# Performance work log

Hardware: AMD Instinct MI355X
Metric: run time of the kernel (lower is better)

The kernel has to match this reference:

```python
import jax, jax.numpy as jnp
import numpy as np

N = 2000
E = 20000
C = 16
B = 128
N_IN = 200   # first N_IN nodes are input nodes
N_OUT = 200  # last N_OUT nodes are output nodes
EPS = 1e-5


def setup_inputs() -> dict:
    key = jax.random.key(0)
    ks = jax.random.split(key, 8)
    x = jax.random.normal(ks[0], (B, N), dtype=jnp.float32)
    edge_index = jax.random.randint(ks[1], (2, E), 0, N, dtype=jnp.int32)
    input_node_mask = jnp.arange(N) < N_IN
    output_node_mask = jnp.arange(N) >= (N - N_OUT)
    func_mask = ~(input_node_mask | output_node_mask)
    # sparse-linear parameters (structured forms of W1/W2/W3)
    w1 = jax.random.normal(ks[2], (E, C), dtype=jnp.float32) * (1.0 / np.sqrt(C))
    b1 = jnp.zeros((N, C), dtype=jnp.float32)
    w2 = jax.random.normal(ks[3], (N, C, C), dtype=jnp.float32) * (1.0 / np.sqrt(C))
    b2 = jnp.zeros((N, C), dtype=jnp.float32)
    w3 = jax.random.normal(ks[4], (E, C), dtype=jnp.float32) * 1.0  # d=1 init scale
    b3 = jnp.zeros((E,), dtype=jnp.float32)
    g1 = jnp.ones((N * C,), dtype=jnp.float32)
    be1 = jnp.zeros((N * C,), dtype=jnp.float32)
    g2 = jnp.ones((N * C,), dtype=jnp.float32)
    be2 = jnp.zeros((N * C,), dtype=jnp.float32)
    return {"x": x, "w1": w1, "b1": b1, "w2": w2, "b2": b2, "w3": w3, "b3": b3,
            "g1": g1, "be1": be1, "g2": g2, "be2": be2,
            "edge_index": edge_index, "func_mask": func_mask,
            "output_node_mask": output_node_mask, "layers": 4}


def _batchnorm(h, g, b):
    # training-mode BatchNorm1d: batch mean and biased variance over axis 0
    m = h.mean(axis=0)
    v = h.var(axis=0)
    return (h - m) * jax.lax.rsqrt(v + EPS) * g + b


def reference(x, w1, b1, w2, b2, w3, b3, g1, be1, g2, be2,
              edge_index, func_mask, output_node_mask, layers):
    src, dst = edge_index[0], edge_index[1]
    Bsz, Nn = x.shape
    Ee, Cc = w1.shape
    fm = func_mask.astype(x.dtype)
    w2m = w2 * fm[:, None, None]          # W2 blocks exist only at function nodes
    w3m = w3 * fm[src][:, None]           # W3 rows exist only for edges with src in function nodes

    x0 = x[:, src]                        # node2edge: (B, E)
    xe = x0
    for _ in range(layers):
        # lin1: scatter edge values into dst node hidden channels
        contrib = xe.T[:, :, None] * w1[:, None, :]                    # (E, B, C)
        h = jax.ops.segment_sum(contrib, dst, num_segments=Nn)         # (N, B, C)
        h = jnp.transpose(h, (1, 0, 2)) + b1                           # (B, N, C)
        h = _batchnorm(h.reshape(Bsz, Nn * Cc), g1, be1)
        h = jax.nn.elu(h).reshape(Bsz, Nn, Cc)
        # lin2: block-diagonal C x C mix per (function) node
        h = jnp.einsum('bnc,ncd->bnd', h, w2m) + b2
        h = _batchnorm(h.reshape(Bsz, Nn * Cc), g2, be2)
        h = jax.nn.elu(h).reshape(Bsz, Nn, Cc)
        # lin3: gather src hidden, per-edge dot back to edge space
        xe = jnp.einsum('bec,ec->be', h[:, src], w3m) + b3             # (B, E)
        xe = xe + x0
    # edge2node: scatter-sum edge values to dst nodes, keep output nodes
    nodes = jax.ops.segment_sum(xe.T, dst, num_segments=Nn)            # (N, B)
    return nodes.T * output_node_mask.astype(x.dtype)
```

## Files before the change

kernel.cpp:

```cpp
#include <hip/hip_runtime.h>
#include <math.h>

#define BB 128
#define NN 2000
#define EE 20000
#define CC 16
#define FUNC_LO 200
#define FUNC_HI 1800
#define OUT_LO 1800
#define LAYERS 4
#define EPSV 1e-5f
#define CH 32
#define HP 129


__global__ void k_hist2(const int* __restrict__ ei, int* __restrict__ deg) {
    int e = blockIdx.x * 256 + threadIdx.x;
    if (e < EE) {
        atomicAdd(&deg[ei[EE + e]], 1);
        atomicAdd(&deg[NN + ei[e]], 1);
    }
}

__global__ void k_scan(const int* __restrict__ deg, int* __restrict__ rs,
                       int* __restrict__ cursor) {
    const int PER = 16;
    int tid = threadIdx.x;
    int vals[PER];
    int s = 0;
    #pragma unroll
    for (int i = 0; i < PER; i++) {
        int idx = tid * PER + i;
        int d = (idx < 2 * NN) ? deg[idx] : 0;
        vals[i] = s;
        s += d;
    }
    __shared__ int ts[256];
    ts[tid] = s;
    __syncthreads();
    for (int off = 1; off < 256; off <<= 1) {
        int v = (tid >= off) ? ts[tid - off] : 0;
        __syncthreads();
        ts[tid] += v;
        __syncthreads();
    }
    int base = (tid == 0) ? 0 : ts[tid - 1];
    #pragma unroll
    for (int i = 0; i < PER; i++) {
        int idx = tid * PER + i;
        if (idx < 2 * NN) {
            int v = base + vals[i];
            rs[idx] = v;
            cursor[idx] = v;
        }
    }
    if (tid == 255) rs[2 * NN] = ts[255];
}

__global__ void k_scatter2(const int* __restrict__ ei, int* __restrict__ cursor,
                           int* __restrict__ csr) {
    int e = blockIdx.x * 256 + threadIdx.x;
    if (e < EE) {
        int p = atomicAdd(&cursor[ei[EE + e]], 1);
        csr[p] = e;
        int q = atomicAdd(&cursor[NN + ei[e]], 1);
        csr[q] = e;
    }
}

__global__ void k_transpose(const float* __restrict__ x, float* __restrict__ xT) {
    int idx = blockIdx.x * 256 + threadIdx.x;
    if (idx < BB * NN) {
        int b = idx / NN;
        int n = idx - b * NN;
        xT[n * BB + b] = x[idx];
    }
}

__global__ __launch_bounds__(256) void k_layer(
    const float* __restrict__ xe_in,
    const int* __restrict__ srcmap,
    const float* __restrict__ xT,
    const float* __restrict__ w1, const float* __restrict__ w2,
    const float* __restrict__ w3, const float* __restrict__ b3,
    const float* __restrict__ g1, const float* __restrict__ be1,
    const float* __restrict__ g2, const float* __restrict__ be2,
    const int* __restrict__ rs, const int* __restrict__ csr,
    const int* __restrict__ dstmap,
    float* __restrict__ xe_out)
{
    int n = blockIdx.x;
    int tid = threadIdx.x;
    int b = tid & 127;
    int half = tid >> 7;

    __shared__ float lds_h[CC * HP];
    __shared__ float lds_w2[256];
    __shared__ float lds_w[CH * CC];
    __shared__ int   lds_e[CH];
    __shared__ int   lds_roff[CH];
    __shared__ float lds_bias[CH];
    __shared__ int   lds_wr[CH];
    __shared__ float red_s[256], red_ss[256];
    __shared__ float sc[CC], sh[CC];

    const bool isfunc = (n >= FUNC_LO && n < FUNC_HI);
    float x0r = xT[n * BB + b];

    if (isfunc) {
        lds_w2[tid] = w2[n * 256 + tid];

        float acc[CC];
        #pragma unroll
        for (int c = 0; c < CC; c++) acc[c] = 0.0f;

        int st = rs[n], en = rs[n + 1];
        for (int k0 = st; k0 < en; k0 += CH) {
            int m = min(CH, en - k0);
            if (tid < m) {
                int e = csr[k0 + tid];
                lds_e[tid] = e;
                lds_roff[tid] = (srcmap ? srcmap[e] : e) * BB;
            }
            __syncthreads();
            for (int idx = tid; idx < m * CC; idx += 256)
                lds_w[idx] = w1[(size_t)lds_e[idx >> 4] * CC + (idx & 15)];
            __syncthreads();
            for (int k = half; k < m; k += 2) {
                float v = xe_in[lds_roff[k] + b];
                const float* wr = &lds_w[k * CC];
                #pragma unroll
                for (int c = 0; c < CC; c++) acc[c] += v * wr[c];
            }
            __syncthreads();
        }

        if (half) {
            #pragma unroll
            for (int c = 0; c < CC; c++) lds_h[c * HP + b] = acc[c];
        }
        __syncthreads();
        if (!half) {
            #pragma unroll
            for (int c = 0; c < CC; c++) lds_h[c * HP + b] += acc[c];
        }
        __syncthreads();

        {
            int c = tid & 15, r = tid >> 4;
            float s = 0.f, ss = 0.f;
            #pragma unroll
            for (int i = 0; i < 8; i++) {
                float v = lds_h[c * HP + r * 8 + i];
                s += v; ss += v * v;
            }
            red_s[tid] = s; red_ss[tid] = ss;
        }
        __syncthreads();
        if (tid < CC) {
            float S = 0.f, SS = 0.f;
            #pragma unroll
            for (int r = 0; r < 16; r++) { S += red_s[r * 16 + tid]; SS += red_ss[r * 16 + tid]; }
            float mean = S * (1.0f / 128.0f);
            float var = SS * (1.0f / 128.0f) - mean * mean;
            float scale = rsqrtf(var + EPSV) * g1[n * CC + tid];
            sc[tid] = scale;
            sh[tid] = be1[n * CC + tid] - mean * scale;
        }
        __syncthreads();

        for (int idx = tid; idx < CC * BB; idx += 256) {
            int c = idx >> 7, b2 = idx & 127;
            float a = lds_h[c * HP + b2] * sc[c] + sh[c];
            a = (a > 0.0f) ? a : (__expf(a) - 1.0f);
            lds_h[c * HP + b2] = a;
        }
        __syncthreads();

        int d = tid & 15, brow = tid >> 4;
        float h2[8];
        #pragma unroll
        for (int j = 0; j < 8; j++) {
            float a2 = 0.f;
            #pragma unroll
            for (int c = 0; c < CC; c++)
                a2 += lds_h[c * HP + brow + 16 * j] * lds_w2[c * 16 + d];
            h2[j] = a2;
        }

        float s = 0.f, ss = 0.f;
        #pragma unroll
        for (int j = 0; j < 8; j++) { s += h2[j]; ss += h2[j] * h2[j]; }
        red_s[tid] = s; red_ss[tid] = ss;
        __syncthreads();
        if (tid < CC) {
            float S = 0.f, SS = 0.f;
            #pragma unroll
            for (int r = 0; r < 16; r++) { S += red_s[r * 16 + tid]; SS += red_ss[r * 16 + tid]; }
            float mean = S * (1.0f / 128.0f);
            float var = SS * (1.0f / 128.0f) - mean * mean;
            float scale = rsqrtf(var + EPSV) * g2[n * CC + tid];
            sc[tid] = scale;
            sh[tid] = be2[n * CC + tid] - mean * scale;
        }
        __syncthreads();

        #pragma unroll
        for (int j = 0; j < 8; j++) {
            float a = h2[j] * sc[d] + sh[d];
            a = (a > 0.0f) ? a : (__expf(a) - 1.0f);
            lds_h[d * HP + brow + 16 * j] = a;
        }
        __syncthreads();
    }

    int st2 = rs[NN + n], en2 = rs[NN + n + 1];
    const bool last = (dstmap != nullptr);
    for (int k0 = st2; k0 < en2; k0 += CH) {
        int m = min(CH, en2 - k0);
        if (tid < m) {
            int e = csr[EE + 0 + k0 + tid - EE];
            e = csr[k0 + tid];
            lds_e[tid] = e;
            lds_bias[tid] = b3[e];
            lds_wr[tid] = last ? (dstmap[e] >= OUT_LO ? 1 : 0) : 1;
        }
        __syncthreads();
        if (isfunc) {
            for (int idx = tid; idx < m * CC; idx += 256)
                lds_w[idx] = w3[(size_t)lds_e[idx >> 4] * CC + (idx & 15)];
        }
        __syncthreads();
        for (int k = half; k < m; k += 2) {
            if (!lds_wr[k]) continue;
            float dot = 0.f;
            if (isfunc) {
                const float* wr = &lds_w[k * CC];
                #pragma unroll
                for (int d2 = 0; d2 < CC; d2++) dot += lds_h[d2 * HP + b] * wr[d2];
            }
            xe_out[(size_t)lds_e[k] * BB + b] = dot + lds_bias[k] + x0r;
        }
        __syncthreads();
    }
}

__global__ void k_out(const float* __restrict__ xe, const int* __restrict__ rs,
                      const int* __restrict__ csr, float* __restrict__ out)
{
    int n = OUT_LO + blockIdx.x;
    int b = threadIdx.x;
    int st = rs[n], en = rs[n + 1];
    float s = 0.f;
    for (int k = st; k < en; k++) {
        int e = csr[k];
        s += xe[(size_t)e * BB + b];
    }
    out[(size_t)b * NN + n] = s;
}

extern "C" void kernel_launch(void* const* d_in, const int* in_sizes, int n_in,
                              void* d_out, int out_size, void* d_ws, size_t ws_size,
                              hipStream_t stream) {
    const float* x   = (const float*)d_in[0];
    const float* w1  = (const float*)d_in[1];
    const float* w2  = (const float*)d_in[3];
    const float* w3  = (const float*)d_in[5];
    const float* b3  = (const float*)d_in[6];
    const float* g1  = (const float*)d_in[7];
    const float* be1 = (const float*)d_in[8];
    const float* g2  = (const float*)d_in[9];
    const float* be2 = (const float*)d_in[10];
    const int* ei    = (const int*)d_in[11];
    const int* srcp  = ei;
    const int* dstp  = ei + EE;
    float* out = (float*)d_out;

    char* ws = (char*)d_ws;
    float* xT  = (float*)ws;  ws += (size_t)NN * BB * 4;
    float* xeA = (float*)ws;  ws += (size_t)EE * BB * 4;
    float* xeB = (float*)ws;  ws += (size_t)EE * BB * 4;
    int* deg    = (int*)ws;   ws += (size_t)2 * NN * 4;
    int* rs     = (int*)ws;   ws += (size_t)(2 * NN + 1) * 4 + 12;
    int* cursor = (int*)ws;   ws += (size_t)2 * NN * 4;
    int* csr    = (int*)ws;   ws += (size_t)2 * EE * 4;

    hipMemsetAsync(deg, 0, 2 * NN * sizeof(int), stream);
    k_hist2<<<(EE + 255) / 256, 256, 0, stream>>>(ei, deg);
    k_scan<<<1, 256, 0, stream>>>(deg, rs, cursor);
    k_scatter2<<<(EE + 255) / 256, 256, 0, stream>>>(ei, cursor, csr);
    k_transpose<<<(NN * BB + 255) / 256, 256, 0, stream>>>(x, xT);

    k_layer<<<NN, 256, 0, stream>>>(xT,  srcp,    xT, w1, w2, w3, b3, g1, be1, g2, be2, rs, csr, nullptr, xeA);
    k_layer<<<NN, 256, 0, stream>>>(xeA, nullptr, xT, w1, w2, w3, b3, g1, be1, g2, be2, rs, csr, nullptr, xeB);
    k_layer<<<NN, 256, 0, stream>>>(xeB, nullptr, xT, w1, w2, w3, b3, g1, be1, g2, be2, rs, csr, nullptr, xeA);
    k_layer<<<NN, 256, 0, stream>>>(xeA, nullptr, xT, w1, w2, w3, b3, g1, be1, g2, be2, rs, csr, dstp,    xeB);

    hipMemsetAsync(d_out, 0, (size_t)out_size * sizeof(float), stream);
    k_out<<<NN - OUT_LO, BB, 0, stream>>>(xeB, rs, csr, out);
}
```

Baseline: 203.4 us.

## Presort edge weights and store edge activations in dst-CSR order

Adds a presort kernel that copies w1, w3 and b3 into CSR order and precomputes write offsets, so the lin1 gather reads edge activations contiguously in dst-sorted order with no csr indirection. lin3 now writes each edge value to its dst-CSR position. The final layer accumulates output nodes directly with atomics into a small transposed buffer, which replaces the separate k_out gather. Setup kernels are merged into one prep kernel, the output memset is removed, and the chunk size is doubled. The cost is one extra presort pass, and the output sum now relies on float atomics.

```diff
diff --git a/kernel.cpp b/kernel.cpp
--- a/kernel.cpp
+++ b/kernel.cpp
@@ -8,18 +8,23 @@
 #define FUNC_LO 200
 #define FUNC_HI 1800
 #define OUT_LO 1800
-#define LAYERS 4
+#define OUTN 200
 #define EPSV 1e-5f
-#define CH 32
+#define CH 64
 #define HP 129
 
-
-__global__ void k_hist2(const int* __restrict__ ei, int* __restrict__ deg) {
-    int e = blockIdx.x * 256 + threadIdx.x;
-    if (e < EE) {
-        atomicAdd(&deg[ei[EE + e]], 1);
-        atomicAdd(&deg[NN + ei[e]], 1);
-    }
+__global__ void k_prep1(const float* __restrict__ x, float* __restrict__ xT,
+                        const int* __restrict__ ei, int* __restrict__ deg,
+                        float* __restrict__ outT) {
+    int idx = blockIdx.x * 256 + threadIdx.x;
+    if (idx < EE) {
+        atomicAdd(&deg[ei[EE + idx]], 1);
+        atomicAdd(&deg[NN + ei[idx]], 1);
+    }
+    if (idx < OUTN * BB) outT[idx] = 0.0f;
+    int b = idx / NN;
+    int n = idx - b * NN;
+    if (idx < BB * NN) xT[n * BB + b] = x[idx];
 }
 
 __global__ void k_scan(const int* __restrict__ deg, int* __restrict__ rs,
@@ -58,36 +63,53 @@
 }
 
 __global__ void k_scatter2(const int* __restrict__ ei, int* __restrict__ cursor,
-                           int* __restrict__ csr) {
+                           int* __restrict__ csr, int* __restrict__ pos) {
     int e = blockIdx.x * 256 + threadIdx.x;
     if (e < EE) {
         int p = atomicAdd(&cursor[ei[EE + e]], 1);
         csr[p] = e;
+        pos[e] = p;
         int q = atomicAdd(&cursor[NN + ei[e]], 1);
         csr[q] = e;
     }
 }
 
-__global__ void k_transpose(const float* __restrict__ x, float* __restrict__ xT) {
-    int idx = blockIdx.x * 256 + threadIdx.x;
-    if (idx < BB * NN) {
-        int b = idx / NN;
-        int n = idx - b * NN;
-        xT[n * BB + b] = x[idx];
+__global__ void k_presort(const int* __restrict__ ei, const int* __restrict__ csr,
+                          const int* __restrict__ pos,
+                          const float* __restrict__ w1, const float* __restrict__ w3,
+                          const float* __restrict__ b3,
+                          float* __restrict__ w1s, float* __restrict__ w3s,
+                          float* __restrict__ b3s, int* __restrict__ row0s,
+                          int* __restrict__ wout, int* __restrict__ dsts) {
+    int t = blockIdx.x * 256 + threadIdx.x;
+    if (t < EE * CC) {
+        int k = t >> 4, c = t & 15;
+        w1s[t] = w1[(size_t)csr[k] * CC + c];
+        w3s[t] = w3[(size_t)csr[EE + k] * CC + c];
+    }
+    if (t < EE) {
+        int e1 = csr[t];
+        row0s[t] = ei[e1] * BB;
+        int e2 = csr[EE + t];
+        b3s[t]  = b3[e2];
+        wout[t] = pos[e2] * BB;
+        dsts[t] = ei[EE + e2];
     }
 }
 
 __global__ __launch_bounds__(256) void k_layer(
     const float* __restrict__ xe_in,
-    const int* __restrict__ srcmap,
+    const int* __restrict__ row0s,
     const float* __restrict__ xT,
-    const float* __restrict__ w1, const float* __restrict__ w2,
-    const float* __restrict__ w3, const float* __restrict__ b3,
+    const float* __restrict__ w1s, const float* __restrict__ w2,
+    const float* __restrict__ w3s, const float* __restrict__ b3s,
+    const int* __restrict__ wout,
     const float* __restrict__ g1, const float* __restrict__ be1,
     const float* __restrict__ g2, const float* __restrict__ be2,
-    const int* __restrict__ rs, const int* __restrict__ csr,
-    const int* __restrict__ dstmap,
-    float* __restrict__ xe_out)
+    const int* __restrict__ rs,
+    const int* __restrict__ dsts,
+    float* __restrict__ xe_out,
+    float* __restrict__ outT)
 {
     int n = blockIdx.x;
     int tid = threadIdx.x;
@@ -97,10 +119,8 @@
     __shared__ float lds_h[CC * HP];
     __shared__ float lds_w2[256];
     __shared__ float lds_w[CH * CC];
-    __shared__ int   lds_e[CH];
-    __shared__ int   lds_roff[CH];
-    __shared__ float lds_bias[CH];
-    __shared__ int   lds_wr[CH];
+    __shared__ int   lds_i[CH];
+    __shared__ float lds_b[CH];
     __shared__ float red_s[256], red_ss[256];
     __shared__ float sc[CC], sh[CC];
 
@@ -117,17 +137,13 @@
         int st = rs[n], en = rs[n + 1];
         for (int k0 = st; k0 < en; k0 += CH) {
             int m = min(CH, en - k0);
-            if (tid < m) {
-                int e = csr[k0 + tid];
-                lds_e[tid] = e;
-                lds_roff[tid] = (srcmap ? srcmap[e] : e) * BB;
-            }
-            __syncthreads();
             for (int idx = tid; idx < m * CC; idx += 256)
-                lds_w[idx] = w1[(size_t)lds_e[idx >> 4] * CC + (idx & 15)];
+                lds_w[idx] = w1s[(size_t)k0 * CC + idx];
+            if (row0s && tid < m) lds_i[tid] = row0s[k0 + tid];
             __syncthreads();
             for (int k = half; k < m; k += 2) {
-                float v = xe_in[lds_roff[k] + b];
+                int off = row0s ? lds_i[k] : (k0 + k) * BB;
+                float v = xe_in[off + b];
                 const float* wr = &lds_w[k * CC];
                 #pragma unroll
                 for (int c = 0; c < CC; c++) acc[c] += v * wr[c];
@@ -214,49 +230,48 @@
         __syncthreads();
     }
 
-    int st2 = rs[NN + n], en2 = rs[NN + n + 1];
-    const bool last = (dstmap != nullptr);
+    int st2 = rs[NN + n] - EE, en2 = rs[NN + n + 1] - EE;
+    const bool last = (dsts != nullptr);
     for (int k0 = st2; k0 < en2; k0 += CH) {
         int m = min(CH, en2 - k0);
         if (tid < m) {
-            int e = csr[EE + 0 + k0 + tid - EE];
-            e = csr[k0 + tid];
-            lds_e[tid] = e;
-            lds_bias[tid] = b3[e];
-            lds_wr[tid] = last ? (dstmap[e] >= OUT_LO ? 1 : 0) : 1;
-        }
-        __syncthreads();
+            lds_b[tid] = b3s[k0 + tid];
+            if (last) {
+                int dn = dsts[k0 + tid];
+                lds_i[tid] = (dn >= OUT_LO) ? (dn - OUT_LO) * BB : -1;
+            } else {
+                lds_i[tid] = wout[k0 + tid];
+            }
+        }
         if (isfunc) {
             for (int idx = tid; idx < m * CC; idx += 256)
-                lds_w[idx] = w3[(size_t)lds_e[idx >> 4] * CC + (idx & 15)];
+                lds_w[idx] = w3s[(size_t)k0 * CC + idx];
         }
         __syncthreads();
         for (int k = half; k < m; k += 2) {
-            if (!lds_wr[k]) continue;
+            int o = lds_i[k];
+            if (last && o < 0) continue;
             float dot = 0.f;
             if (isfunc) {
                 const float* wr = &lds_w[k * CC];
                 #pragma unroll
                 for (int d2 = 0; d2 < CC; d2++) dot += lds_h[d2 * HP + b] * wr[d2];
             }
-            xe_out[(size_t)lds_e[k] * BB + b] = dot + lds_bias[k] + x0r;
-        }
-        __syncthreads();
-    }
-}
-
-__global__ void k_out(const float* __restrict__ xe, const int* __restrict__ rs,
-                      const int* __restrict__ csr, float* __restrict__ out)
-{
-    int n = OUT_LO + blockIdx.x;
-    int b = threadIdx.x;
-    int st = rs[n], en = rs[n + 1];
-    float s = 0.f;
-    for (int k = st; k < en; k++) {
-        int e = csr[k];
-        s += xe[(size_t)e * BB + b];
-    }
-    out[(size_t)b * NN + n] = s;
+            float val = dot + lds_b[k] + x0r;
+            if (last) atomicAdd(&outT[o + b], val);
+            else      xe_out[o + b] = val;
+        }
+        __syncthreads();
+    }
+}
+
+__global__ void k_finalize(const float* __restrict__ outT, float* __restrict__ out) {
+    int idx = blockIdx.x * 256 + threadIdx.x;
+    if (idx < BB * NN) {
+        int b = idx / NN;
+        int n = idx - b * NN;
+        out[idx] = (n >= OUT_LO) ? outT[(n - OUT_LO) * BB + b] : 0.0f;
+    }
 }
 
 extern "C" void kernel_launch(void* const* d_in, const int* in_sizes, int n_in,
@@ -272,30 +287,40 @@
     const float* g2  = (const float*)d_in[9];
     const float* be2 = (const float*)d_in[10];
     const int* ei    = (const int*)d_in[11];
-    const int* srcp  = ei;
-    const int* dstp  = ei + EE;
     float* out = (float*)d_out;
 
     char* ws = (char*)d_ws;
-    float* xT  = (float*)ws;  ws += (size_t)NN * BB * 4;
-    float* xeA = (float*)ws;  ws += (size_t)EE * BB * 4;
-    float* xeB = (float*)ws;  ws += (size_t)EE * BB * 4;
-    int* deg    = (int*)ws;   ws += (size_t)2 * NN * 4;
-    int* rs     = (int*)ws;   ws += (size_t)(2 * NN + 1) * 4 + 12;
-    int* cursor = (int*)ws;   ws += (size_t)2 * NN * 4;
-    int* csr    = (int*)ws;   ws += (size_t)2 * EE * 4;
+    float* xT   = (float*)ws;  ws += (size_t)NN * BB * 4;
+    float* xeA  = (float*)ws;  ws += (size_t)EE * BB * 4;
+    float* xeB  = (float*)ws;  ws += (size_t)EE * BB * 4;
+    float* w1s  = (float*)ws;  ws += (size_t)EE * CC * 4;
+    float* w3s  = (float*)ws;  ws += (size_t)EE * CC * 4;
+    float* b3s  = (float*)ws;  ws += (size_t)EE * 4;
+    float* outT = (float*)ws;  ws += (size_t)OUTN * BB * 4;
+    int* deg    = (int*)ws;    ws += (size_t)2 * NN * 4;
+    int* rs     = (int*)ws;    ws += (size_t)(2 * NN + 1) * 4 + 12;
+    int* cursor = (int*)ws;    ws += (size_t)2 * NN * 4;
+    int* csr    = (int*)ws;    ws += (size_t)2 * EE * 4;
+    int* pos    = (int*)ws;    ws += (size_t)EE * 4;
+    int* row0s  = (int*)ws;    ws += (size_t)EE * 4;
+    int* wout   = (int*)ws;    ws += (size_t)EE * 4;
+    int* dsts   = (int*)ws;    ws += (size_t)EE * 4;
 
     hipMemsetAsync(deg, 0, 2 * NN * sizeof(int), stream);
-    k_hist2<<<(EE + 255) / 256, 256, 0, stream>>>(ei, deg);
+    k_prep1<<<(NN * BB) / 256, 256, 0, stream>>>(x, xT, ei, deg, outT);
     k_scan<<<1, 256, 0, stream>>>(deg, rs, cursor);
-    k_scatter2<<<(EE + 255) / 256, 256, 0, stream>>>(ei, cursor, csr);
-    k_transpose<<<(NN * BB + 255) / 256, 256, 0, stream>>>(x, xT);
-
-    k_layer<<<NN, 256, 0, stream>>>(xT,  srcp,    xT, w1, w2, w3, b3, g1, be1, g2, be2, rs, csr, nullptr, xeA);
-    k_layer<<<NN, 256, 0, stream>>>(xeA, nullptr, xT, w1, w2, w3, b3, g1, be1, g2, be2, rs, csr, nullptr, xeB);
-    k_layer<<<NN, 256, 0, stream>>>(xeB, nullptr, xT, w1, w2, w3, b3, g1, be1, g2, be2, rs, csr, nullptr, xeA);
-    k_layer<<<NN, 256, 0, stream>>>(xeA, nullptr, xT, w1, w2, w3, b3, g1, be1, g2, be2, rs, csr, dstp,    xeB);
-
-    hipMemsetAsync(d_out, 0, (size_t)out_size * sizeof(float), stream);
-    k_out<<<NN - OUT_LO, BB, 0, stream>>>(xeB, rs, csr, out);
-}
+    k_scatter2<<<(EE + 255) / 256, 256, 0, stream>>>(ei, cursor, csr, pos);
+    k_presort<<<(EE * CC) / 256, 256, 0, stream>>>(ei, csr, pos, w1, w3, b3,
+                                                   w1s, w3s, b3s, row0s, wout, dsts);
+
+    k_layer<<<NN, 256, 0, stream>>>(xT,  row0s,   xT, w1s, w2, w3s, b3s, wout,
+                                    g1, be1, g2, be2, rs, nullptr, xeA, outT);
+    k_layer<<<NN, 256, 0, stream>>>(xeA, nullptr, xT, w1s, w2, w3s, b3s, wout,
+                                    g1, be1, g2, be2, rs, nullptr, xeB, outT);
+    k_layer<<<NN, 256, 0, stream>>>(xeB, nullptr, xT, w1s, w2, w3s, b3s, wout,
+                                    g1, be1, g2, be2, rs, nullptr, xeA, outT);
+    k_layer<<<NN, 256, 0, stream>>>(xeA, nullptr, xT, w1s, w2, w3s, b3s, wout,
+                                    g1, be1, g2, be2, rs, dsts,    xeB, outT);
+
+    k_finalize<<<(NN * BB) / 256, 256, 0, stream>>>(outT, out);
+}
```

New measurement: 195.7 us. 3.8% less time.
